# Optimization experiments

Hardware: AMD Instinct MI355X
Metric: run time of the kernel (lower is better)

The kernel has to match this reference:

```python
import jax, jax.numpy as jnp
import numpy as np

B, S, DM = 8, 1024, 512   # batch, seq_len, model dim
H, D = 8, 64              # n_heads, per-head dim


def setup_inputs() -> dict:
    key = jax.random.key(0)
    k1, k2, k3, k4, k5 = jax.random.split(key, 5)
    sc = 1.0 / np.sqrt(DM)
    return {
        "x": jax.random.normal(k1, (B, S, DM), dtype=jnp.float32),
        "Wq": jax.random.normal(k2, (H, DM, D), dtype=jnp.float32) * sc,
        "Wk": jax.random.normal(k3, (H, DM, D), dtype=jnp.float32) * sc,
        "Wv": jax.random.normal(k4, (H, DM, D), dtype=jnp.float32) * sc,
        "Wo": jax.random.normal(k5, (H * D, DM), dtype=jnp.float32) * (1.0 / np.sqrt(H * D)),
    }


def reference(x, Wq, Wk, Wv, Wo):
    # Batched multi-head attention equivalent to the per-head Python loop.
    q = jnp.einsum("bsm,hmd->bhsd", x, Wq)
    k = jnp.einsum("bsm,hmd->bhsd", x, Wk)
    v = jnp.einsum("bsm,hmd->bhsd", x, Wv)
    scores = jnp.einsum("bhsd,bhtd->bhst", q, k) / jnp.sqrt(jnp.float32(D))
    attn = jax.nn.softmax(scores, axis=-1)          # [B,H,S,S]
    heads = jnp.einsum("bhst,bhtd->bhsd", attn, v)  # [B,H,S,D]
    # concat heads along feature dim (head order matches loop order)
    concat = heads.transpose(0, 2, 1, 3).reshape(B, S, H * D)
    z = jnp.einsum("bsf,fm->bsm", concat, Wo)       # output projection
    return z, attn
```

## Files before the change

kernel.cpp:

```cpp
#include <hip/hip_runtime.h>

#define B 8
#define S 1024
#define DM 512
#define H 8
#define D 64

typedef __attribute__((ext_vector_type(8))) short bf16x8;
typedef __attribute__((ext_vector_type(4))) float f32x4;

__device__ inline f32x4 mfma16(bf16x8 a, bf16x8 b, f32x4 c) {
  return __builtin_amdgcn_mfma_f32_16x16x32_bf16(a, b, c, 0, 0, 0);
}

__device__ inline ushort f2bf(float f) {
  uint u = __float_as_uint(f);
  u += 0x7fff + ((u >> 16) & 1);
  return (ushort)(u >> 16);
}

__device__ inline float bf2f(ushort u) {
  return __uint_as_float(((uint)u) << 16);
}

__global__ __launch_bounds__(256) void cast_x_kernel(const float* __restrict__ x,
                                                     ushort* __restrict__ xbf) {
  int idx = blockIdx.x * 256 + threadIdx.x;
  float4 v = *(const float4*)(x + (size_t)idx * 4);
  ushort4 o;
  o.x = f2bf(v.x); o.y = f2bf(v.y); o.z = f2bf(v.z); o.w = f2bf(v.w);
  *(ushort4*)(xbf + (size_t)idx * 4) = o;
}

__global__ __launch_bounds__(256) void prep_w_kernel(
    const float* __restrict__ Wq, const float* __restrict__ Wk,
    const float* __restrict__ Wv, const float* __restrict__ Wo,
    ushort* __restrict__ WT, ushort* __restrict__ WoT) {
  int idx = blockIdx.x * 256 + threadIdx.x;
  if (idx < 1536 * 512) {
    int f = idx >> 9, m = idx & 511;
    int g = f >> 9, fl = f & 511, h = fl >> 6, d = fl & 63;
    const float* W = (g == 0) ? Wq : (g == 1) ? Wk : Wv;
    WT[idx] = f2bf(W[((size_t)h * DM + m) * D + d]);
  } else {
    int i2 = idx - 1536 * 512;
    int m = i2 >> 9, f = i2 & 511;
    WoT[(size_t)m * 512 + f] = f2bf(Wo[(size_t)f * DM + m]);
  }
}

__global__ __launch_bounds__(256) void qkv_gemm_kernel(
    const ushort* __restrict__ A, const ushort* __restrict__ Bm,
    ushort* __restrict__ qb, ushort* __restrict__ kb, ushort* __restrict__ vt) {
  __shared__ ushort As[64][72], Bs[64][72];
  const int tid = threadIdx.x;
  const int m0 = blockIdx.x * 64, n0 = blockIdx.y * 64;
  const int w = tid >> 6, l = tid & 63;
  const int r = l & 15, q = l >> 4;
  const int mh = (w >> 1) * 32, nh = (w & 1) * 32;

  f32x4 acc[2][2] = {};
  const int srow = tid >> 2, sco = (tid & 3) * 16;

  for (int k0 = 0; k0 < 512; k0 += 64) {
    const ushort* ap = A + (size_t)(m0 + srow) * 512 + k0 + sco;
    const ushort* bp = Bm + (size_t)(n0 + srow) * 512 + k0 + sco;
    uint4 a0 = *(const uint4*)ap;
    uint4 a1 = *(const uint4*)(ap + 8);
    uint4 b0 = *(const uint4*)bp;
    uint4 b1 = *(const uint4*)(bp + 8);
    __syncthreads();
    *(uint4*)&As[srow][sco] = a0;
    *(uint4*)&As[srow][sco + 8] = a1;
    *(uint4*)&Bs[srow][sco] = b0;
    *(uint4*)&Bs[srow][sco + 8] = b1;
    __syncthreads();
    #pragma unroll
    for (int kk = 0; kk < 64; kk += 32) {
      bf16x8 fa0 = *(const bf16x8*)&As[mh + r][kk + q * 8];
      bf16x8 fa1 = *(const bf16x8*)&As[mh + 16 + r][kk + q * 8];
      bf16x8 fb0 = *(const bf16x8*)&Bs[nh + r][kk + q * 8];
      bf16x8 fb1 = *(const bf16x8*)&Bs[nh + 16 + r][kk + q * 8];
      acc[0][0] = mfma16(fa0, fb0, acc[0][0]);
      acc[0][1] = mfma16(fa0, fb1, acc[0][1]);
      acc[1][0] = mfma16(fa1, fb0, acc[1][0]);
      acc[1][1] = mfma16(fa1, fb1, acc[1][1]);
    }
  }

  const int g = n0 >> 9;
  #pragma unroll
  for (int mi = 0; mi < 2; ++mi)
    #pragma unroll
    for (int nj = 0; nj < 2; ++nj)
      #pragma unroll
      for (int i = 0; i < 4; ++i) {
        int row = m0 + mh + mi * 16 + q * 4 + i;
        int col = n0 + nh + nj * 16 + r;
        int bb = row >> 10, s = row & 1023;
        int fl = col & 511, h = fl >> 6, d = fl & 63;
        ushort val = f2bf(acc[mi][nj][i]);
        if (g == 0)
          qb[(((size_t)bb * H + h) * S + s) * D + d] = val;
        else if (g == 1)
          kb[(((size_t)bb * H + h) * S + s) * D + d] = val;
        else
          vt[(((size_t)bb * H + h) * D + d) * S + s] = val;
      }
}

__global__ __launch_bounds__(256, 4) void attn_kernel(
    const ushort* __restrict__ qb, const ushort* __restrict__ kb,
    const ushort* __restrict__ vt, float* __restrict__ attn,
    ushort* __restrict__ concat) {
  __shared__ ushort Pl[16 * 1024];
  __shared__ float redsum[4][16];
  __shared__ float rinvL[16];
  const int tid = threadIdx.x;
  const int w = tid >> 6, l = tid & 63;
  const int r = l & 15, q = l >> 4;

  const int n = blockIdx.x;
  const int rank = n >> 3;
  const int bh = (n & 7) * 8 + (rank >> 6);
  const int s0 = (rank & 63) * 16;

  const ushort* qp = qb + ((size_t)bh * S + s0) * D;
  bf16x8 qa0 = *(const bf16x8*)(qp + r * 64 + q * 8);
  bf16x8 qa1 = *(const bf16x8*)(qp + r * 64 + 32 + q * 8);

  const ushort* kp = kb + (size_t)bh * S * D;
  f32x4 sc[16];
  float sm[4] = {0.f, 0.f, 0.f, 0.f};
  #pragma unroll
  for (int kt = 0; kt < 16; ++kt) {
    const ushort* kr = kp + (size_t)(w * 256 + kt * 16 + r) * 64 + q * 8;
    bf16x8 kf0 = *(const bf16x8*)kr;
    bf16x8 kf1 = *(const bf16x8*)(kr + 32);
    f32x4 a = {};
    a = mfma16(qa0, kf0, a);
    a = mfma16(qa1, kf1, a);
    #pragma unroll
    for (int i = 0; i < 4; ++i) {
      float e = __expf(a[i] * 0.125f);
      sc[kt][i] = e;
      sm[i] += e;
    }
  }

  #pragma unroll
  for (int i = 0; i < 4; ++i) {
    float s = sm[i];
    #pragma unroll
    for (int msk = 1; msk < 16; msk <<= 1) s += __shfl_xor(s, msk);
    sm[i] = s;
  }
  if (r == 0) {
    #pragma unroll
    for (int i = 0; i < 4; ++i) redsum[w][q * 4 + i] = sm[i];
  }
  __syncthreads();
  float rinv[4];
  #pragma unroll
  for (int i = 0; i < 4; ++i)
    rinv[i] = 1.0f / (redsum[0][q * 4 + i] + redsum[1][q * 4 + i] +
                      redsum[2][q * 4 + i] + redsum[3][q * 4 + i]);
  if (w == 0 && r == 0) {
    #pragma unroll
    for (int i = 0; i < 4; ++i) rinvL[q * 4 + i] = rinv[i];
  }

  #pragma unroll
  for (int kt = 0; kt < 16; ++kt) {
    int col = w * 256 + kt * 16 + r;
    #pragma unroll
    for (int i = 0; i < 4; ++i) {
      int row = q * 4 + i;
      Pl[row * 1024 + (col ^ ((row & 7) << 3))] = f2bf(sc[kt][i]);
    }
  }
  __syncthreads();

  {
    const int d0 = w * 16;
    const ushort* vp = vt + ((size_t)bh * D + d0 + r) * S;
    f32x4 acc[4] = {};
    #pragma unroll
    for (int stp = 0; stp < 32; ++stp) {
      int t0 = stp * 32 + q * 8;
      bf16x8 pa = *(const bf16x8*)&Pl[r * 1024 + (t0 ^ ((r & 7) << 3))];
      bf16x8 vb = *(const bf16x8*)(vp + t0);
      acc[stp & 3] = mfma16(pa, vb, acc[stp & 3]);
    }
    f32x4 tot = acc[0] + acc[1] + acc[2] + acc[3];
    const int b = bh >> 3, h = bh & 7;
    #pragma unroll
    for (int i = 0; i < 4; ++i)
      concat[((size_t)b * S + s0 + q * 4 + i) * DM + h * D + d0 + r] =
          f2bf(tot[i] * rinv[i]);
  }

  {
    float* ap = attn + ((size_t)bh * S + s0) * S;
    #pragma unroll
    for (int uu = 0; uu < 16; ++uu) {
      const int row = w * 4 + (uu >> 2);
      const int chunk = uu & 3;
      const int c = chunk * 256 + l * 4;
      const int swz = (row & 7) << 3;
      ushort4 p4 = *(const ushort4*)&Pl[row * 1024 + (c ^ swz)];
      const float rv = rinvL[row];
      f32x4 o;
      o.x = bf2f(p4.x) * rv;
      o.y = bf2f(p4.y) * rv;
      o.z = bf2f(p4.z) * rv;
      o.w = bf2f(p4.w) * rv;
      __builtin_nontemporal_store(o, (f32x4*)(ap + (size_t)row * S + c));
    }
  }
}

__global__ __launch_bounds__(256) void outproj_gemm_kernel(
    const ushort* __restrict__ A, const ushort* __restrict__ Bm,
    float* __restrict__ z) {
  __shared__ ushort As[64][72], Bs[64][72];
  const int tid = threadIdx.x;
  const int m0 = blockIdx.x * 64, n0 = blockIdx.y * 64;
  const int w = tid >> 6, l = tid & 63;
  const int r = l & 15, q = l >> 4;
  const int mh = (w >> 1) * 32, nh = (w & 1) * 32;

  f32x4 acc[2][2] = {};
  const int srow = tid >> 2, sco = (tid & 3) * 16;

  for (int k0 = 0; k0 < 512; k0 += 64) {
    const ushort* ap = A + (size_t)(m0 + srow) * 512 + k0 + sco;
    const ushort* bp = Bm + (size_t)(n0 + srow) * 512 + k0 + sco;
    uint4 a0 = *(const uint4*)ap;
    uint4 a1 = *(const uint4*)(ap + 8);
    uint4 b0 = *(const uint4*)bp;
    uint4 b1 = *(const uint4*)(bp + 8);
    __syncthreads();
    *(uint4*)&As[srow][sco] = a0;
    *(uint4*)&As[srow][sco + 8] = a1;
    *(uint4*)&Bs[srow][sco] = b0;
    *(uint4*)&Bs[srow][sco + 8] = b1;
    __syncthreads();
    #pragma unroll
    for (int kk = 0; kk < 64; kk += 32) {
      bf16x8 fa0 = *(const bf16x8*)&As[mh + r][kk + q * 8];
      bf16x8 fa1 = *(const bf16x8*)&As[mh + 16 + r][kk + q * 8];
      bf16x8 fb0 = *(const bf16x8*)&Bs[nh + r][kk + q * 8];
      bf16x8 fb1 = *(const bf16x8*)&Bs[nh + 16 + r][kk + q * 8];
      acc[0][0] = mfma16(fa0, fb0, acc[0][0]);
      acc[0][1] = mfma16(fa0, fb1, acc[0][1]);
      acc[1][0] = mfma16(fa1, fb0, acc[1][0]);
      acc[1][1] = mfma16(fa1, fb1, acc[1][1]);
    }
  }

  #pragma unroll
  for (int mi = 0; mi < 2; ++mi)
    #pragma unroll
    for (int nj = 0; nj < 2; ++nj)
      #pragma unroll
      for (int i = 0; i < 4; ++i) {
        int row = m0 + mh + mi * 16 + q * 4 + i;
        int col = n0 + nh + nj * 16 + r;
        z[(size_t)row * DM + col] = acc[mi][nj][i];
      }
}

extern "C" void kernel_launch(void* const* d_in, const int* in_sizes, int n_in,
                              void* d_out, int out_size, void* d_ws, size_t ws_size,
                              hipStream_t stream) {
  const float* x  = (const float*)d_in[0];
  const float* Wq = (const float*)d_in[1];
  const float* Wk = (const float*)d_in[2];
  const float* Wv = (const float*)d_in[3];
  const float* Wo = (const float*)d_in[4];

  float* z    = (float*)d_out;
  float* attn = z + (size_t)B * S * DM;

  ushort* xbf    = (ushort*)d_ws;
  ushort* WT     = xbf + (size_t)8192 * 512;
  ushort* WoT    = WT + (size_t)1536 * 512;
  ushort* qb     = WoT + (size_t)512 * 512;
  ushort* kb     = qb + (size_t)B * H * S * D;
  ushort* vt     = kb + (size_t)B * H * S * D;
  ushort* concat = vt + (size_t)B * H * S * D;

  cast_x_kernel<<<(B * S * DM / 4 + 255) / 256, 256, 0, stream>>>(x, xbf);
  prep_w_kernel<<<(1536 * 512 + 512 * 512) / 256, 256, 0, stream>>>(
      Wq, Wk, Wv, Wo, WT, WoT);
  qkv_gemm_kernel<<<dim3(8192 / 64, 1536 / 64), 256, 0, stream>>>(
      xbf, WT, qb, kb, vt);
  attn_kernel<<<4096, 256, 0, stream>>>(qb, kb, vt, attn, concat);
  outproj_gemm_kernel<<<dim3(8192 / 64, 512 / 64), 256, 0, stream>>>(
      concat, WoT, z);
}
```

Measured before the change: 185.8 us.

## Transpose score MFMA to store attn directly from registers in fp32

Swaps the MFMA operand order so each lane holds four consecutive key columns of one query row. The row-sum now needs only two cross-lane shuffles, P can be written to LDS as packed ushort4, and the fp32 attention probabilities are stored straight from registers instead of being re-read from bf16 LDS. This removes an LDS readback pass, one barrier's worth of work and the bf16 round-trip on the attn output, which also improves its precision. The per-lane global stores become 16-byte chunks strided by row, which may coalesce less well than the previous contiguous per-row stores.

```diff
diff --git a/kernel.cpp b/kernel.cpp
--- a/kernel.cpp
+++ b/kernel.cpp
@@ -115,7 +115,6 @@
     ushort* __restrict__ concat) {
   __shared__ ushort Pl[16 * 1024];
   __shared__ float redsum[4][16];
-  __shared__ float rinvL[16];
   const int tid = threadIdx.x;
   const int w = tid >> 6, l = tid & 63;
   const int r = l & 15, q = l >> 4;
@@ -130,56 +129,57 @@
   bf16x8 qa1 = *(const bf16x8*)(qp + r * 64 + 32 + q * 8);
 
   const ushort* kp = kb + (size_t)bh * S * D;
-  f32x4 sc[16];
-  float sm[4] = {0.f, 0.f, 0.f, 0.f};
+  f32x4 p[16];
+  float sm = 0.f;
   #pragma unroll
   for (int kt = 0; kt < 16; ++kt) {
     const ushort* kr = kp + (size_t)(w * 256 + kt * 16 + r) * 64 + q * 8;
     bf16x8 kf0 = *(const bf16x8*)kr;
     bf16x8 kf1 = *(const bf16x8*)(kr + 32);
     f32x4 a = {};
-    a = mfma16(qa0, kf0, a);
-    a = mfma16(qa1, kf1, a);
+    a = mfma16(kf0, qa0, a);
+    a = mfma16(kf1, qa1, a);
     #pragma unroll
     for (int i = 0; i < 4; ++i) {
       float e = __expf(a[i] * 0.125f);
-      sc[kt][i] = e;
-      sm[i] += e;
-    }
-  }
-
+      p[kt][i] = e;
+      sm += e;
+    }
+  }
+
+  sm += __shfl_xor(sm, 16);
+  sm += __shfl_xor(sm, 32);
+  if (q == 0) redsum[w][r] = sm;
+
+  #pragma unroll
+  for (int kt = 0; kt < 16; ++kt) {
+    int col = w * 256 + kt * 16 + q * 4;
+    ushort4 pk;
+    pk.x = f2bf(p[kt][0]); pk.y = f2bf(p[kt][1]);
+    pk.z = f2bf(p[kt][2]); pk.w = f2bf(p[kt][3]);
+    *(ushort4*)&Pl[r * 1024 + (col ^ ((r & 7) << 3))] = pk;
+  }
+  __syncthreads();
+
+  float rinv_r = 1.0f / (redsum[0][r] + redsum[1][r] +
+                         redsum[2][r] + redsum[3][r]);
+  float rpv[4];
   #pragma unroll
   for (int i = 0; i < 4; ++i) {
-    float s = sm[i];
-    #pragma unroll
-    for (int msk = 1; msk < 16; msk <<= 1) s += __shfl_xor(s, msk);
-    sm[i] = s;
-  }
-  if (r == 0) {
-    #pragma unroll
-    for (int i = 0; i < 4; ++i) redsum[w][q * 4 + i] = sm[i];
-  }
-  __syncthreads();
-  float rinv[4];
-  #pragma unroll
-  for (int i = 0; i < 4; ++i)
-    rinv[i] = 1.0f / (redsum[0][q * 4 + i] + redsum[1][q * 4 + i] +
-                      redsum[2][q * 4 + i] + redsum[3][q * 4 + i]);
-  if (w == 0 && r == 0) {
-    #pragma unroll
-    for (int i = 0; i < 4; ++i) rinvL[q * 4 + i] = rinv[i];
-  }
-
-  #pragma unroll
-  for (int kt = 0; kt < 16; ++kt) {
-    int col = w * 256 + kt * 16 + r;
-    #pragma unroll
-    for (int i = 0; i < 4; ++i) {
-      int row = q * 4 + i;
-      Pl[row * 1024 + (col ^ ((row & 7) << 3))] = f2bf(sc[kt][i]);
-    }
-  }
-  __syncthreads();
+    int rr = q * 4 + i;
+    rpv[i] = 1.0f / (redsum[0][rr] + redsum[1][rr] +
+                     redsum[2][rr] + redsum[3][rr]);
+  }
+
+  {
+    float* ap = attn + ((size_t)bh * S + s0) * S;
+    #pragma unroll
+    for (int kt = 0; kt < 16; ++kt) {
+      f32x4 o = p[kt] * rinv_r;
+      __builtin_nontemporal_store(
+          o, (f32x4*)(ap + (size_t)r * S + w * 256 + kt * 16 + q * 4));
+    }
+  }
 
   {
     const int d0 = w * 16;
@@ -197,26 +197,7 @@
     #pragma unroll
     for (int i = 0; i < 4; ++i)
       concat[((size_t)b * S + s0 + q * 4 + i) * DM + h * D + d0 + r] =
-          f2bf(tot[i] * rinv[i]);
-  }
-
-  {
-    float* ap = attn + ((size_t)bh * S + s0) * S;
-    #pragma unroll
-    for (int uu = 0; uu < 16; ++uu) {
-      const int row = w * 4 + (uu >> 2);
-      const int chunk = uu & 3;
-      const int c = chunk * 256 + l * 4;
-      const int swz = (row & 7) << 3;
-      ushort4 p4 = *(const ushort4*)&Pl[row * 1024 + (c ^ swz)];
-      const float rv = rinvL[row];
-      f32x4 o;
-      o.x = bf2f(p4.x) * rv;
-      o.y = bf2f(p4.y) * rv;
-      o.z = bf2f(p4.z) * rv;
-      o.w = bf2f(p4.w) * rv;
-      __builtin_nontemporal_store(o, (f32x4*)(ap + (size_t)row * S + c));
-    }
+          f2bf(tot[i] * rpv[i]);
   }
 }
 
```

New measurement: 192.9 us. +3.9%, slower.
